# Optimization experiments

Hardware: AMD Instinct MI355X
Metric: run time of the kernel (lower is better)

Reference implementation:

```python
import jax, jax.numpy as jnp
import numpy as np

B, S, NX, H = 8, 1024, 1024, 16
D = NX // H  # head_features = 64
SCALE = True


def setup_inputs() -> dict:
    key = jax.random.key(0)
    k1, k2, k3 = jax.random.split(key, 3)
    x = jax.random.normal(k1, (B, S, NX), dtype=jnp.float32)
    w_attn = jax.random.normal(k2, (NX, 3 * NX), dtype=jnp.float32) * 0.02
    b_attn = jnp.zeros((3 * NX,), dtype=jnp.float32)
    w_proj = jax.random.normal(k3, (NX, NX), dtype=jnp.float32) * 0.02
    b_proj = jnp.zeros((NX,), dtype=jnp.float32)
    return {"x": x, "w_attn": w_attn, "b_attn": b_attn, "w_proj": w_proj, "b_proj": b_proj}


def _split_heads(t):
    # (B, S, NX) -> (B, H, S, D)
    return t.reshape(B, S, H, D).transpose(0, 2, 1, 3)


def reference(x, w_attn, b_attn, w_proj, b_proj):
    # fused QKV projection (Conv1D): addmm over flattened tokens
    qkv = x @ w_attn + b_attn                      # (B, S, 3*NX)
    q, k, v = jnp.split(qkv, 3, axis=-1)
    q = _split_heads(q)                            # (B, H, S, D)
    k = _split_heads(k)
    v = _split_heads(v)

    w = jnp.einsum("bhqd,bhkd->bhqk", q, k)        # full S x S scores
    if SCALE:
        w = w / jnp.sqrt(jnp.asarray(D, w.dtype))
    # causal mask applied exactly as in the source: multiply + big-negative subtract
    b = jnp.tril(jnp.ones((S, S), dtype=w.dtype))[None, None]
    w = w * b - 1e10 * (1.0 - b)
    w = jax.nn.softmax(w, axis=-1)                 # attn_pdrop = 0 (eval)
    a = jnp.einsum("bhqk,bhkd->bhqd", w, v)        # (B, H, S, D)

    # merge heads: (B, H, S, D) -> (B, S, NX)
    a = a.transpose(0, 2, 1, 3).reshape(B, S, NX)
    a = a @ w_proj + b_proj                        # c_proj; resid_pdrop = 0 (eval)
    return a
```

## Files before the change

### kernel.cpp

```cpp
#include <hip/hip_runtime.h>
#include <hip/hip_bf16.h>

#define BB 8
#define SS 1024
#define NXX 1024
#define HH 16
#define DD 64
#define MM (BB * SS)

typedef __attribute__((ext_vector_type(8))) short short8;
typedef __attribute__((ext_vector_type(4))) short short4v;
typedef __attribute__((ext_vector_type(4))) float float4v;

static __device__ inline short bf16bits(float v) {
    __hip_bfloat16 t = __float2bfloat16(v);
    return *reinterpret_cast<short*>(&t);
}

__global__ __launch_bounds__(256) void prep_kernel(
    const float* __restrict__ x, __hip_bfloat16* __restrict__ xb,
    const float* __restrict__ w_attn, __hip_bfloat16* __restrict__ wT_attn,
    const float* __restrict__ w_proj, __hip_bfloat16* __restrict__ wT_proj)
{
    __shared__ __hip_bfloat16 tile[32][33];
    const int blk = blockIdx.x;
    const int tid = threadIdx.x;

    if (blk < 8192) {
        int i = blk * 1024 + tid * 4;
        float4 v = *(const float4*)(x + i);
        xb[i + 0] = __float2bfloat16(v.x);
        xb[i + 1] = __float2bfloat16(v.y);
        xb[i + 2] = __float2bfloat16(v.z);
        xb[i + 3] = __float2bfloat16(v.w);
        return;
    }
    const float* W;
    __hip_bfloat16* Wt;
    int K, N, idx;
    if (blk < 8192 + 3072) { idx = blk - 8192;  W = w_attn; Wt = wT_attn; K = NXX; N = 3 * NXX; }
    else                   { idx = blk - 11264; W = w_proj; Wt = wT_proj; K = NXX; N = NXX; }
    const int k0 = (idx % (K / 32)) * 32;
    const int n0 = (idx / (K / 32)) * 32;
    const int tx = tid % 32;
    const int ty = tid / 32;
#pragma unroll
    for (int p = 0; p < 4; ++p) {
        int k = ty + p * 8;
        tile[k][tx] = __float2bfloat16(W[(size_t)(k0 + k) * N + n0 + tx]);
    }
    __syncthreads();
#pragma unroll
    for (int p = 0; p < 4; ++p) {
        int nn = ty + p * 8;
        Wt[(size_t)(n0 + nn) * K + k0 + tx] = tile[tx][nn];
    }
}

template <int MODE>
__global__ __launch_bounds__(256) void gemm_bf16_mfma(
    const __hip_bfloat16* __restrict__ A,
    const __hip_bfloat16* __restrict__ Bt,
    const float* __restrict__ bias,
    void* __restrict__ Cv,
    __hip_bfloat16* __restrict__ vT,
    int M, int K, int N)
{
    __shared__ __hip_bfloat16 As[128 * 32];
    __shared__ __hip_bfloat16 Bs[128 * 32];

    const int tid  = threadIdx.x;
    const int wave = tid >> 6;
    const int lane = tid & 63;
    const int m0 = blockIdx.x * 128;
    const int n0 = blockIdx.y * 128;
    const int wm = (wave & 1) * 64;
    const int wn = (wave >> 1) * 64;

    float4v acc[4][4];
#pragma unroll
    for (int i = 0; i < 4; ++i)
#pragma unroll
        for (int j = 0; j < 4; ++j) acc[i][j] = (float4v){0.f, 0.f, 0.f, 0.f};

    const int fr = lane & 15;
    const int fk = (lane >> 4) * 8;

    const short* AsS = (const short*)As;
    const short* BsS = (const short*)Bs;

    for (int k0 = 0; k0 < K; k0 += 32) {
#pragma unroll
        for (int j = 0; j < 2; ++j) {
            int c = j * 256 + tid;
            int row = c >> 2;
            int kk = (c & 3) * 8;
            const __hip_bfloat16* ga = A + (size_t)(m0 + row) * K + k0 + kk;
            const __hip_bfloat16* gb = Bt + (size_t)(n0 + row) * K + k0 + kk;
            char* la = (char*)As + j * 4096 + (wave << 10);
            char* lb = (char*)Bs + j * 4096 + (wave << 10);
            __builtin_amdgcn_global_load_lds(
                (const __attribute__((address_space(1))) void*)ga,
                (__attribute__((address_space(3))) void*)la, 16, 0, 0);
            __builtin_amdgcn_global_load_lds(
                (const __attribute__((address_space(1))) void*)gb,
                (__attribute__((address_space(3))) void*)lb, 16, 0, 0);
        }
        __syncthreads();

        short8 a_frag[4], b_frag[4];
#pragma unroll
        for (int i = 0; i < 4; ++i) {
            a_frag[i] = *(const short8*)(AsS + (wm + i * 16 + fr) * 32 + fk);
            b_frag[i] = *(const short8*)(BsS + (wn + i * 16 + fr) * 32 + fk);
        }
#pragma unroll
        for (int i = 0; i < 4; ++i)
#pragma unroll
            for (int j = 0; j < 4; ++j)
                acc[i][j] = __builtin_amdgcn_mfma_f32_16x16x32_bf16(
                    a_frag[i], b_frag[j], acc[i][j], 0, 0, 0);
        __syncthreads();
    }

    const int cr = (lane >> 4) * 4;
    const int cc = lane & 15;

    if (MODE == 1 && n0 >= 2048) {
        const int bb = m0 / SS;
#pragma unroll
        for (int i = 0; i < 4; ++i) {
            int grow = m0 + wm + i * 16 + cr;
            int ssr = grow & (SS - 1);
#pragma unroll
            for (int j = 0; j < 4; ++j) {
                int gcol = n0 + wn + j * 16 + cc;
                float bv = bias[gcol];
                int col = gcol - 2048;
                int hh = col >> 6, dd = col & 63;
                short4v pk;
#pragma unroll
                for (int r = 0; r < 4; ++r) pk[r] = bf16bits(acc[i][j][r] + bv);
                *(short4v*)(vT + (size_t)((bb * HH + hh) * 64 + dd) * SS + ssr) = pk;
            }
        }
    } else {
        const float qs = (MODE == 1 && n0 < 1024) ? 0.125f : 1.0f;
#pragma unroll
        for (int i = 0; i < 4; ++i) {
            int grow = m0 + wm + i * 16 + cr;
#pragma unroll
            for (int j = 0; j < 4; ++j) {
                int gcol = n0 + wn + j * 16 + cc;
                float bv = bias[gcol];
#pragma unroll
                for (int r = 0; r < 4; ++r) {
                    float v = (acc[i][j][r] + bv) * qs;
                    if constexpr (MODE == 1)
                        ((__hip_bfloat16*)Cv)[(size_t)(grow + r) * N + gcol] =
                            __float2bfloat16(v);
                    else
                        ((float*)Cv)[(size_t)(grow + r) * N + gcol] = v;
                }
            }
        }
    }
}

#define PSTR 72

__global__ __launch_bounds__(256) void attn_mfma_kernel(
    const __hip_bfloat16* __restrict__ qkv,
    const __hip_bfloat16* __restrict__ vT,
    __hip_bfloat16* __restrict__ aout)
{
    const int bh = blockIdx.x;
    const int b = bh / HH, h = bh % HH;
    const int q0 = ((int)gridDim.y - 1 - (int)blockIdx.y) * 128;

    __shared__ __hip_bfloat16 Ks[64 * PSTR];
    __shared__ __hip_bfloat16 Vs[64 * PSTR];
    __shared__ __hip_bfloat16 Ps[4][32 * PSTR];

    const int tid  = threadIdx.x;
    const int wave = tid >> 6;
    const int lane = tid & 63;
    const int quad = lane >> 4;
    const int l16  = lane & 15;

    short8 qf[2][2];
#pragma unroll
    for (int t = 0; t < 2; ++t) {
        const __hip_bfloat16* qp = qkv +
            (size_t)(b * SS + q0 + wave * 32 + t * 16 + l16) * 3072 + h * 64 + quad * 8;
        qf[t][0] = *(const short8*)qp;
        qf[t][1] = *(const short8*)(qp + 32);
    }

    float4v o_acc[2][4];
    float l_acc[2][4];
#pragma unroll
    for (int t = 0; t < 2; ++t)
#pragma unroll
        for (int nt = 0; nt < 4; ++nt) o_acc[t][nt] = (float4v){0.f, 0.f, 0.f, 0.f};
#pragma unroll
    for (int t = 0; t < 2; ++t)
#pragma unroll
        for (int r = 0; r < 4; ++r) l_acc[t][r] = 0.f;

    const int sk  = tid & 63;
    const int sdo = (tid >> 6) * 16;
    const int vd  = tid >> 2;
    const int vko = (tid & 3) * 16;
    const int qmin_w = q0 + wave * 32;
    const int nkt = q0 / 64 + 2;

    for (int kt = 0; kt < nkt; ++kt) {
        const int k0 = kt * 64;
        __syncthreads();
        {
            const __hip_bfloat16* kr =
                qkv + (size_t)(b * SS + k0 + sk) * 3072 + 1024 + h * 64 + sdo;
            *(short8*)&Ks[sk * PSTR + sdo]     = *(const short8*)kr;
            *(short8*)&Ks[sk * PSTR + sdo + 8] = *(const short8*)(kr + 8);
            const __hip_bfloat16* vr = vT + (size_t)(bh * 64 + vd) * SS + k0 + vko;
            *(short8*)&Vs[vd * PSTR + vko]     = *(const short8*)vr;
            *(short8*)&Vs[vd * PSTR + vko + 8] = *(const short8*)(vr + 8);
        }
        __syncthreads();
        if (k0 > qmin_w + 31) continue;

        const short* ks = (const short*)Ks;
        float4v sacc[2][4];
#pragma unroll
        for (int t = 0; t < 2; ++t)
#pragma unroll
            for (int nt = 0; nt < 4; ++nt) sacc[t][nt] = (float4v){0.f, 0.f, 0.f, 0.f};
#pragma unroll
        for (int kc = 0; kc < 2; ++kc)
#pragma unroll
            for (int nt = 0; nt < 4; ++nt) {
                short8 kb = *(const short8*)(ks + (nt * 16 + l16) * PSTR + kc * 32 + quad * 8);
                sacc[0][nt] = __builtin_amdgcn_mfma_f32_16x16x32_bf16(qf[0][kc], kb, sacc[0][nt], 0, 0, 0);
                sacc[1][nt] = __builtin_amdgcn_mfma_f32_16x16x32_bf16(qf[1][kc], kb, sacc[1][nt], 0, 0, 0);
            }

        const bool needmask = (k0 + 63 > qmin_w);
        __hip_bfloat16* pw = Ps[wave];
#pragma unroll
        for (int t = 0; t < 2; ++t)
#pragma unroll
            for (int nt = 0; nt < 4; ++nt) {
                int kk = k0 + nt * 16 + l16;
#pragma unroll
                for (int r = 0; r < 4; ++r) {
                    float s = sacc[t][nt][r];
                    if (needmask) {
                        int qq = qmin_w + t * 16 + quad * 4 + r;
                        if (kk > qq) s = -1e10f;
                    }
                    float p = __expf(s);
                    l_acc[t][r] += p;
                    pw[(t * 16 + quad * 4 + r) * PSTR + nt * 16 + l16] =
                        __float2bfloat16(p);
                }
            }

        const short* ps = (const short*)pw;
        const short* vs = (const short*)Vs;
#pragma unroll
        for (int kc = 0; kc < 2; ++kc) {
            short8 pa0 = *(const short8*)(ps + (0 * 16 + l16) * PSTR + kc * 32 + quad * 8);
            short8 pa1 = *(const short8*)(ps + (1 * 16 + l16) * PSTR + kc * 32 + quad * 8);
#pragma unroll
            for (int nt = 0; nt < 4; ++nt) {
                short8 vb = *(const short8*)(vs + (nt * 16 + l16) * PSTR + kc * 32 + quad * 8);
                o_acc[0][nt] = __builtin_amdgcn_mfma_f32_16x16x32_bf16(pa0, vb, o_acc[0][nt], 0, 0, 0);
                o_acc[1][nt] = __builtin_amdgcn_mfma_f32_16x16x32_bf16(pa1, vb, o_acc[1][nt], 0, 0, 0);
            }
        }
    }

#pragma unroll
    for (int t = 0; t < 2; ++t)
#pragma unroll
        for (int r = 0; r < 4; ++r) {
            float l = l_acc[t][r];
            l += __shfl_xor(l, 1);
            l += __shfl_xor(l, 2);
            l += __shfl_xor(l, 4);
            l += __shfl_xor(l, 8);
            float inv = 1.f / l;
            int row = q0 + wave * 32 + t * 16 + quad * 4 + r;
            __hip_bfloat16* op = aout + (size_t)(b * SS + row) * NXX + h * 64 + l16;
#pragma unroll
            for (int nt = 0; nt < 4; ++nt)
                op[nt * 16] = __float2bfloat16(o_acc[t][nt][r] * inv);
        }
}

extern "C" void kernel_launch(void* const* d_in, const int* in_sizes, int n_in,
                              void* d_out, int out_size, void* d_ws, size_t ws_size,
                              hipStream_t stream)
{
    const float* x      = (const float*)d_in[0];
    const float* w_attn = (const float*)d_in[1];
    const float* b_attn = (const float*)d_in[2];
    const float* w_proj = (const float*)d_in[3];
    const float* b_proj = (const float*)d_in[4];
    float* out = (float*)d_out;

    char* ws = (char*)d_ws;
    __hip_bfloat16* qkv     = (__hip_bfloat16*)ws;
    __hip_bfloat16* vT      = (__hip_bfloat16*)(ws + (size_t)48 * 1024 * 1024);
    __hip_bfloat16* xb      = (__hip_bfloat16*)(ws + (size_t)64 * 1024 * 1024);
    __hip_bfloat16* amid    = xb;
    __hip_bfloat16* wT_attn = (__hip_bfloat16*)(ws + (size_t)80 * 1024 * 1024);
    __hip_bfloat16* wT_proj = (__hip_bfloat16*)(ws + (size_t)86 * 1024 * 1024);

    dim3 blk(256);

    prep_kernel<<<dim3(12288), blk, 0, stream>>>(
        x, xb, w_attn, wT_attn, w_proj, wT_proj);

    gemm_bf16_mfma<1><<<dim3(MM / 128, (3 * NXX) / 128), blk, 0, stream>>>(
        xb, wT_attn, b_attn, qkv, vT, MM, NXX, 3 * NXX);

    attn_mfma_kernel<<<dim3(BB * HH, SS / 128), blk, 0, stream>>>(qkv, vT, amid);

    gemm_bf16_mfma<0><<<dim3(MM / 128, NXX / 128), blk, 0, stream>>>(
        amid, wT_proj, b_proj, out, nullptr, MM, NXX, NXX);
}
```

Before: 247.8 us.

## Split V transpose into separate kernel, fold Q scale into weights, shrink proj tile

The QKV GEMM no longer writes V transposed with scattered 8-byte stores; it writes plain row-major bf16 output, and a new kernel transposes V through LDS with 16-byte stores. The 1/8 query scale is folded into the weight conversion and a prescaled bias buffer, which removes the per-element multiply in the epilogue. The output projection GEMM gets its own kernel with 64-row tiles, doubling the block count for better occupancy and load balance. In exchange this adds one kernel launch and an extra read and write of V.

```diff
diff --git a/kernel.cpp b/kernel.cpp
--- a/kernel.cpp
+++ b/kernel.cpp
@@ -9,18 +9,13 @@
 #define MM (BB * SS)
 
 typedef __attribute__((ext_vector_type(8))) short short8;
-typedef __attribute__((ext_vector_type(4))) short short4v;
 typedef __attribute__((ext_vector_type(4))) float float4v;
-
-static __device__ inline short bf16bits(float v) {
-    __hip_bfloat16 t = __float2bfloat16(v);
-    return *reinterpret_cast<short*>(&t);
-}
 
 __global__ __launch_bounds__(256) void prep_kernel(
     const float* __restrict__ x, __hip_bfloat16* __restrict__ xb,
     const float* __restrict__ w_attn, __hip_bfloat16* __restrict__ wT_attn,
-    const float* __restrict__ w_proj, __hip_bfloat16* __restrict__ wT_proj)
+    const float* __restrict__ w_proj, __hip_bfloat16* __restrict__ wT_proj,
+    const float* __restrict__ b_attn, float* __restrict__ bias_s)
 {
     __shared__ __hip_bfloat16 tile[32][33];
     const int blk = blockIdx.x;
@@ -35,19 +30,29 @@
         xb[i + 3] = __float2bfloat16(v.w);
         return;
     }
+    if (blk == 12288) {
+#pragma unroll
+        for (int j = 0; j < 12; ++j) {
+            int c = j * 256 + tid;
+            bias_s[c] = b_attn[c] * (c < 1024 ? 0.125f : 1.0f);
+        }
+        return;
+    }
     const float* W;
     __hip_bfloat16* Wt;
     int K, N, idx;
+    float scale = 1.0f;
     if (blk < 8192 + 3072) { idx = blk - 8192;  W = w_attn; Wt = wT_attn; K = NXX; N = 3 * NXX; }
     else                   { idx = blk - 11264; W = w_proj; Wt = wT_proj; K = NXX; N = NXX; }
     const int k0 = (idx % (K / 32)) * 32;
     const int n0 = (idx / (K / 32)) * 32;
+    if (W == w_attn && n0 < 1024) scale = 0.125f;
     const int tx = tid % 32;
     const int ty = tid / 32;
 #pragma unroll
     for (int p = 0; p < 4; ++p) {
         int k = ty + p * 8;
-        tile[k][tx] = __float2bfloat16(W[(size_t)(k0 + k) * N + n0 + tx]);
+        tile[k][tx] = __float2bfloat16(W[(size_t)(k0 + k) * N + n0 + tx] * scale);
     }
     __syncthreads();
 #pragma unroll
@@ -57,13 +62,11 @@
     }
 }
 
-template <int MODE>
-__global__ __launch_bounds__(256) void gemm_bf16_mfma(
+__global__ __launch_bounds__(256) void gemm_qkv(
     const __hip_bfloat16* __restrict__ A,
     const __hip_bfloat16* __restrict__ Bt,
     const float* __restrict__ bias,
-    void* __restrict__ Cv,
-    __hip_bfloat16* __restrict__ vT,
+    __hip_bfloat16* __restrict__ C,
     int M, int K, int N)
 {
     __shared__ __hip_bfloat16 As[128 * 32];
@@ -85,7 +88,6 @@
 
     const int fr = lane & 15;
     const int fk = (lane >> 4) * 8;
-
     const short* AsS = (const short*)As;
     const short* BsS = (const short*)Bs;
 
@@ -125,44 +127,130 @@
 
     const int cr = (lane >> 4) * 4;
     const int cc = lane & 15;
-
-    if (MODE == 1 && n0 >= 2048) {
-        const int bb = m0 / SS;
-#pragma unroll
-        for (int i = 0; i < 4; ++i) {
-            int grow = m0 + wm + i * 16 + cr;
-            int ssr = grow & (SS - 1);
-#pragma unroll
-            for (int j = 0; j < 4; ++j) {
-                int gcol = n0 + wn + j * 16 + cc;
-                float bv = bias[gcol];
-                int col = gcol - 2048;
-                int hh = col >> 6, dd = col & 63;
-                short4v pk;
-#pragma unroll
-                for (int r = 0; r < 4; ++r) pk[r] = bf16bits(acc[i][j][r] + bv);
-                *(short4v*)(vT + (size_t)((bb * HH + hh) * 64 + dd) * SS + ssr) = pk;
-            }
-        }
-    } else {
-        const float qs = (MODE == 1 && n0 < 1024) ? 0.125f : 1.0f;
-#pragma unroll
-        for (int i = 0; i < 4; ++i) {
-            int grow = m0 + wm + i * 16 + cr;
-#pragma unroll
-            for (int j = 0; j < 4; ++j) {
-                int gcol = n0 + wn + j * 16 + cc;
-                float bv = bias[gcol];
-#pragma unroll
-                for (int r = 0; r < 4; ++r) {
-                    float v = (acc[i][j][r] + bv) * qs;
-                    if constexpr (MODE == 1)
-                        ((__hip_bfloat16*)Cv)[(size_t)(grow + r) * N + gcol] =
-                            __float2bfloat16(v);
-                    else
-                        ((float*)Cv)[(size_t)(grow + r) * N + gcol] = v;
-                }
-            }
+#pragma unroll
+    for (int i = 0; i < 4; ++i) {
+        int grow = m0 + wm + i * 16 + cr;
+#pragma unroll
+        for (int j = 0; j < 4; ++j) {
+            int gcol = n0 + wn + j * 16 + cc;
+            float bv = bias[gcol];
+#pragma unroll
+            for (int r = 0; r < 4; ++r)
+                C[(size_t)(grow + r) * N + gcol] =
+                    __float2bfloat16(acc[i][j][r] + bv);
+        }
+    }
+}
+
+__global__ __launch_bounds__(256) void vtrans_kernel(
+    const __hip_bfloat16* __restrict__ qkv, __hip_bfloat16* __restrict__ vT)
+{
+    __shared__ __hip_bfloat16 Ts[256 * 72];
+    const int bh = blockIdx.x;
+    const int b = bh >> 4, h = bh & 15;
+    const int s0 = blockIdx.y * 256;
+    const int tid = threadIdx.x;
+
+    const __hip_bfloat16* g =
+        qkv + (size_t)(b * SS + s0 + tid) * 3072 + 2048 + h * 64;
+#pragma unroll
+    for (int j = 0; j < 8; ++j)
+        *(short8*)&Ts[tid * 72 + j * 8] = *(const short8*)(g + j * 8);
+    __syncthreads();
+
+    const int d  = tid >> 2;
+    const int sb = (tid & 3) * 64;
+    __hip_bfloat16* o = vT + (size_t)(bh * 64 + d) * SS + s0 + sb;
+#pragma unroll
+    for (int j = 0; j < 8; ++j) {
+        short8 p;
+#pragma unroll
+        for (int i = 0; i < 8; ++i)
+            p[i] = *(const short*)&Ts[(sb + j * 8 + i) * 72 + d];
+        *(short8*)(o + j * 8) = p;
+    }
+}
+
+__global__ __launch_bounds__(256) void gemm_proj(
+    const __hip_bfloat16* __restrict__ A,
+    const __hip_bfloat16* __restrict__ Bt,
+    const float* __restrict__ bias,
+    float* __restrict__ C,
+    int M, int K, int N)
+{
+    __shared__ __hip_bfloat16 As[64 * 32];
+    __shared__ __hip_bfloat16 Bs[128 * 32];
+
+    const int tid  = threadIdx.x;
+    const int wave = tid >> 6;
+    const int lane = tid & 63;
+    const int m0 = blockIdx.x * 64;
+    const int n0 = blockIdx.y * 128;
+    const int wm = (wave & 1) * 32;
+    const int wn = (wave >> 1) * 64;
+
+    float4v acc[2][4];
+#pragma unroll
+    for (int i = 0; i < 2; ++i)
+#pragma unroll
+        for (int j = 0; j < 4; ++j) acc[i][j] = (float4v){0.f, 0.f, 0.f, 0.f};
+
+    const int fr = lane & 15;
+    const int fk = (lane >> 4) * 8;
+    const short* AsS = (const short*)As;
+    const short* BsS = (const short*)Bs;
+
+    for (int k0 = 0; k0 < K; k0 += 32) {
+        {
+            int row = tid >> 2;
+            int kk = (tid & 3) * 8;
+            const __hip_bfloat16* ga = A + (size_t)(m0 + row) * K + k0 + kk;
+            char* la = (char*)As + (wave << 10);
+            __builtin_amdgcn_global_load_lds(
+                (const __attribute__((address_space(1))) void*)ga,
+                (__attribute__((address_space(3))) void*)la, 16, 0, 0);
+        }
+#pragma unroll
+        for (int j = 0; j < 2; ++j) {
+            int c = j * 256 + tid;
+            int row = c >> 2;
+            int kk = (c & 3) * 8;
+            const __hip_bfloat16* gb = Bt + (size_t)(n0 + row) * K + k0 + kk;
+            char* lb = (char*)Bs + j * 4096 + (wave << 10);
+            __builtin_amdgcn_global_load_lds(
+                (const __attribute__((address_space(1))) void*)gb,
+                (__attribute__((address_space(3))) void*)lb, 16, 0, 0);
+        }
+        __syncthreads();
+
+        short8 a_frag[2], b_frag[4];
+#pragma unroll
+        for (int i = 0; i < 2; ++i)
+            a_frag[i] = *(const short8*)(AsS + (wm + i * 16 + fr) * 32 + fk);
+#pragma unroll
+        for (int j = 0; j < 4; ++j)
+            b_frag[j] = *(const short8*)(BsS + (wn + j * 16 + fr) * 32 + fk);
+#pragma unroll
+        for (int i = 0; i < 2; ++i)
+#pragma unroll
+            for (int j = 0; j < 4; ++j)
+                acc[i][j] = __builtin_amdgcn_mfma_f32_16x16x32_bf16(
+                    a_frag[i], b_frag[j], acc[i][j], 0, 0, 0);
+        __syncthreads();
+    }
+
+    const int cr = (lane >> 4) * 4;
+    const int cc = lane & 15;
+#pragma unroll
+    for (int i = 0; i < 2; ++i) {
+        int grow = m0 + wm + i * 16 + cr;
+#pragma unroll
+        for (int j = 0; j < 4; ++j) {
+            int gcol = n0 + wn + j * 16 + cc;
+            float bv = bias[gcol];
+#pragma unroll
+            for (int r = 0; r < 4; ++r)
+                C[(size_t)(grow + r) * N + gcol] = acc[i][j][r] + bv;
         }
     }
 }
@@ -317,17 +405,20 @@
     __hip_bfloat16* amid    = xb;
     __hip_bfloat16* wT_attn = (__hip_bfloat16*)(ws + (size_t)80 * 1024 * 1024);
     __hip_bfloat16* wT_proj = (__hip_bfloat16*)(ws + (size_t)86 * 1024 * 1024);
+    float*          bias_s  = (float*)(ws + (size_t)88 * 1024 * 1024);
 
     dim3 blk(256);
 
-    prep_kernel<<<dim3(12288), blk, 0, stream>>>(
-        x, xb, w_attn, wT_attn, w_proj, wT_proj);
-
-    gemm_bf16_mfma<1><<<dim3(MM / 128, (3 * NXX) / 128), blk, 0, stream>>>(
-        xb, wT_attn, b_attn, qkv, vT, MM, NXX, 3 * NXX);
+    prep_kernel<<<dim3(12289), blk, 0, stream>>>(
+        x, xb, w_attn, wT_attn, w_proj, wT_proj, b_attn, bias_s);
+
+    gemm_qkv<<<dim3(MM / 128, 24), blk, 0, stream>>>(
+        xb, wT_attn, bias_s, qkv, MM, NXX, 3 * NXX);
+
+    vtrans_kernel<<<dim3(BB * HH, SS / 256), blk, 0, stream>>>(qkv, vT);
 
     attn_mfma_kernel<<<dim3(BB * HH, SS / 128), blk, 0, stream>>>(qkv, vT, amid);
 
-    gemm_bf16_mfma<0><<<dim3(MM / 128, NXX / 128), blk, 0, stream>>>(
-        amid, wT_proj, b_proj, out, nullptr, MM, NXX, NXX);
-}
+    gemm_proj<<<dim3(MM / 64, NXX / 128), blk, 0, stream>>>(
+        amid, wT_proj, b_proj, out, MM, NXX, NXX);
+}
```

Measured after the change: 250.4 us. Within noise of the previous version (+1.0%).
